# Kernel optimization log

Hardware: AMD Instinct MI355X
Metric: run time of the kernel (lower is better)

## Reference

```python
import jax, jax.numpy as jnp
import numpy as np

NV, NE = 4096, 8192
FV, FE = 128, 64
FV_OUT = 128


def setup_inputs() -> dict:
    key = jax.random.key(0)
    ks = jax.random.split(key, 8)
    stdv = 1.0 / np.sqrt(FV_OUT)
    return {
        "H_v": jax.random.normal(ks[0], (NV, FV), dtype=jnp.float32),
        "H_e": jax.random.normal(ks[1], (NE, FE), dtype=jnp.float32),
        "adj_e": jax.random.uniform(ks[2], (NE, NE), dtype=jnp.float32),
        "adj_v": jax.random.uniform(ks[3], (NV, NV), dtype=jnp.float32),
        "T": jax.random.uniform(ks[4], (NV, NE), dtype=jnp.float32),
        "weight": jax.random.uniform(ks[5], (FV, FV_OUT), minval=-stdv, maxval=stdv, dtype=jnp.float32),
        "p": jax.random.normal(ks[6], (1, FE), dtype=jnp.float32),
        "bias": jax.random.uniform(ks[7], (FV_OUT,), minval=-stdv, maxval=stdv, dtype=jnp.float32),
    }


def reference(H_v, H_e, adj_e, adj_v, T, weight, p, bias):
    # node_layer=True path of GraphConvolution.forward
    # d = (H_e @ p.T) as a vector over edges; T @ diag(d) == T * d[None, :]
    d = (H_e @ p.T)[:, 0]                       # [Ne]
    multiplier = (T * d[None, :]) @ T.T         # [Nv, Nv]
    n = multiplier.shape[0]
    mask = jnp.eye(n, dtype=multiplier.dtype)   # eye mask: diag -> 1, off-diag -> multiplier
    M1 = mask + (1.0 - mask) * multiplier
    adjusted_A = M1 * adj_v                     # elementwise mask with dense adjacency
    output = adjusted_A @ (H_v @ weight) + bias # [Nv, Fv_out]
    return (output, H_e)
```

## Files before the change

kernel.cpp:

```cpp
#include <hip/hip_runtime.h>
#include <stdint.h>

#define NV 4096
#define NE 8192
#define FV 128
#define FE 64
#define FOUT 128

typedef unsigned short u16;
typedef __attribute__((ext_vector_type(8))) short short8;
typedef __attribute__((ext_vector_type(4))) float f32x4;
typedef __attribute__((ext_vector_type(4))) unsigned short u16x4;

__device__ __forceinline__ u16 f2bf(float f) {
  uint32_t u = __builtin_bit_cast(uint32_t, f);
  u += 0x7fffu + ((u >> 16) & 1u);
  return (u16)(u >> 16);
}
__device__ __forceinline__ float bf2f(u16 h) {
  return __builtin_bit_cast(float, (uint32_t)h << 16);
}

#define AS1(p) ((__attribute__((address_space(1))) void*)(void*)(p))
#define AS3(p) ((__attribute__((address_space(3))) void*)(p))

__global__ __launch_bounds__(256) void k_edge_dot(const float* __restrict__ He,
                                                  const float* __restrict__ p,
                                                  float* __restrict__ d) {
  const int lane = threadIdx.x & 63;
  const int gw = blockIdx.x * 4 + (threadIdx.x >> 6);
  const float pv = p[lane];
  for (int e = gw; e < NE; e += 512) {
    float v = He[(size_t)e * FE + lane] * pv;
    #pragma unroll
    for (int off = 32; off > 0; off >>= 1) v += __shfl_down(v, off);
    if (lane == 0) d[e] = v;
  }
}

__global__ __launch_bounds__(256) void k_convert(const float* __restrict__ T,
                                                 const float* __restrict__ d,
                                                 u16* __restrict__ Ta,
                                                 u16* __restrict__ Tb) {
  size_t idx = ((size_t)blockIdx.x * 256 + threadIdx.x) * 8;
  f32x4 t0 = *(const f32x4*)&T[idx];
  f32x4 t1 = *(const f32x4*)&T[idx + 4];
  int e = (int)(idx & (NE - 1));
  f32x4 d0 = *(const f32x4*)&d[e];
  f32x4 d1 = *(const f32x4*)&d[e + 4];
  short8 a, b;
  a[0] = (short)f2bf(t0.x * d0.x); a[1] = (short)f2bf(t0.y * d0.y);
  a[2] = (short)f2bf(t0.z * d0.z); a[3] = (short)f2bf(t0.w * d0.w);
  a[4] = (short)f2bf(t1.x * d1.x); a[5] = (short)f2bf(t1.y * d1.y);
  a[6] = (short)f2bf(t1.z * d1.z); a[7] = (short)f2bf(t1.w * d1.w);
  b[0] = (short)f2bf(t0.x); b[1] = (short)f2bf(t0.y);
  b[2] = (short)f2bf(t0.z); b[3] = (short)f2bf(t0.w);
  b[4] = (short)f2bf(t1.x); b[5] = (short)f2bf(t1.y);
  b[6] = (short)f2bf(t1.z); b[7] = (short)f2bf(t1.w);
  *(short8*)&Ta[idx] = a;
  *(short8*)&Tb[idx] = b;
}

__global__ __launch_bounds__(256) void k_hw(const float* __restrict__ Hv,
                                            const float* __restrict__ W,
                                            u16* __restrict__ HWt) {
  __shared__ float sW[FV * FOUT];
  __shared__ float sH[8 * FV];
  const int tid = threadIdx.x;
  const int i0 = blockIdx.x * 8;
  #pragma unroll
  for (int k = 0; k < 16; ++k)
    *(f32x4*)&sW[k * 1024 + tid * 4] = *(const f32x4*)&W[k * 1024 + tid * 4];
  *(f32x4*)&sH[tid * 4] = *(const f32x4*)&Hv[(size_t)i0 * FV + tid * 4];
  __syncthreads();
  const int n = tid & 127;
  const int rh = tid >> 7;
  float acc[4] = {0.f, 0.f, 0.f, 0.f};
  #pragma unroll 4
  for (int f = 0; f < FV; ++f) {
    float wv = sW[f * FOUT + n];
    #pragma unroll
    for (int rr = 0; rr < 4; ++rr)
      acc[rr] += sH[(rh * 4 + rr) * FV + f] * wv;
  }
  #pragma unroll
  for (int rr = 0; rr < 4; ++rr)
    HWt[(size_t)n * NV + i0 + rh * 4 + rr] = f2bf(acc[rr]);
}

__global__ __launch_bounds__(256) void k_copy_he(float* __restrict__ out,
                                                 const float* __restrict__ He) {
  size_t idx = ((size_t)blockIdx.x * 256 + threadIdx.x) * 4;
  *(f32x4*)&out[(size_t)NV * FOUT + idx] = *(const f32x4*)&He[idx];
}

__global__ __launch_bounds__(512, 2) void k_gemm_m(const u16* __restrict__ Ta,
                                                   const u16* __restrict__ Tb,
                                                   const float* __restrict__ adjv,
                                                   u16* __restrict__ adjA) {
  __shared__ __align__(16) u16 smem[66560];

  const int bi = blockIdx.x >> 4;
  const int bj = blockIdx.x & 15;
  const int tile_m = bi * 256;
  const int tile_n = bj * 256;
  const int tid = threadIdx.x;
  const int lane = tid & 63;
  const int wid = tid >> 6;
  const int wr = wid >> 2;
  const int wc = wid & 3;
  const int row16 = lane & 15;
  const int quad = lane >> 4;
  const int swz8 = (quad ^ ((row16 >> 1) & 3)) * 8;

  const int srow = tid >> 2;
  const int sslot = (tid & 3) ^ ((tid >> 3) & 3);
  const u16* gA0 = Ta + (size_t)(tile_m + srow) * NE + sslot * 8;
  const u16* gA1 = gA0 + (size_t)128 * NE;
  const u16* gB0 = Tb + (size_t)(tile_n + srow) * NE + sslot * 8;
  const u16* gB1 = gB0 + (size_t)128 * NE;
  const int ldsO0 = (wid * 64) * 8;
  const int ldsO1 = (512 + wid * 64) * 8;

#define STG(gp0, gp1, roff, kcol)                                                                 \
  do {                                                                                            \
    __builtin_amdgcn_global_load_lds(AS1((gp0) + (kcol)), AS3(&smem[(roff) + ldsO0]), 16, 0, 0);  \
    __builtin_amdgcn_global_load_lds(AS1((gp1) + (kcol)), AS3(&smem[(roff) + ldsO1]), 16, 0, 0);  \
  } while (0)

  f32x4 acc[8][4] = {};
  short8 aF[4], bF[4];

  const int arow32 = (wr * 128 + row16) * 32 + swz8;
  const int brow32 = (wc * 64 + row16) * 32 + swz8;

#define LDA4(b, kk, mh)                                                                        \
  do { _Pragma("unroll")                                                                       \
    for (int m2 = 0; m2 < 4; ++m2)                                                             \
      aF[m2] = *(const short8*)&smem[(b)*16384 + (kk)*8192 + arow32 + ((mh)*4 + m2) * 512];    \
  } while (0)

#define LDB4(b, kk)                                                                            \
  do { _Pragma("unroll")                                                                       \
    for (int ni = 0; ni < 4; ++ni)                                                             \
      bF[ni] = *(const short8*)&smem[32768 + (b)*16384 + (kk)*8192 + brow32 + ni * 512];       \
  } while (0)

#define MMH(mh)                                                                                             \
  do { _Pragma("unroll")                                                                                    \
    for (int m2 = 0; m2 < 4; ++m2) { _Pragma("unroll")                                                      \
      for (int ni = 0; ni < 4; ++ni)                                                                        \
        acc[(mh)*4+m2][ni] = __builtin_amdgcn_mfma_f32_16x16x32_bf16(aF[m2], bF[ni], acc[(mh)*4+m2][ni], 0,0,0); \
    }                                                                                                       \
  } while (0)

#define BAR()   __builtin_amdgcn_s_barrier()
#define LGKM0() do { asm volatile("s_waitcnt lgkmcnt(0)" ::: "memory"); \
                     __builtin_amdgcn_sched_barrier(0); } while (0)
#define VM6()   asm volatile("s_waitcnt vmcnt(6)" ::: "memory")
#define PRIO1() __builtin_amdgcn_s_setprio(1)
#define PRIO0() __builtin_amdgcn_s_setprio(0)

  STG(gA0, gA1, 0,     0);
  STG(gB0, gB1, 32768, 0);
  STG(gA0, gA1, 8192,  32);
  STG(gB0, gB1, 40960, 32);
  STG(gB0, gB1, 49152, 64);
  STG(gA0, gA1, 16384, 64);
  STG(gB0, gB1, 57344, 96);
  VM6();
  BAR();

  for (int it = 0; it < 64; ++it) {
    const int t = it * 2;
    const int k1 = (t + 1) * 64;
    const int k2 = (t + 2 < 128 ? t + 2 : 127) * 64;
    const int k3 = (t + 3 < 128 ? t + 3 : 127) * 64;

    LDB4(0, 0); LDA4(0, 0, 0);
    STG(gA0, gA1, 24576, k1 + 32);
    BAR(); LGKM0();
    PRIO1(); MMH(0); PRIO0();
    BAR();

    LDA4(0, 0, 1);
    STG(gB0, gB1, 32768, k2);
    BAR(); LGKM0();
    PRIO1(); MMH(1); PRIO0();
    BAR();

    LDB4(0, 1); LDA4(0, 1, 0);
    STG(gA0, gA1, 0, k2);
    BAR(); LGKM0();
    PRIO1(); MMH(0); PRIO0();
    BAR();

    LDA4(0, 1, 1);
    STG(gB0, gB1, 40960, k2 + 32);
    BAR(); LGKM0();
    PRIO1(); MMH(1); PRIO0();
    VM6();
    BAR();

    LDB4(1, 0); LDA4(1, 0, 0);
    STG(gA0, gA1, 8192, k2 + 32);
    BAR(); LGKM0();
    PRIO1(); MMH(0); PRIO0();
    BAR();

    LDA4(1, 0, 1);
    STG(gB0, gB1, 49152, k3);
    BAR(); LGKM0();
    PRIO1(); MMH(1); PRIO0();
    BAR();

    LDB4(1, 1); LDA4(1, 1, 0);
    STG(gA0, gA1, 16384, k3);
    BAR(); LGKM0();
    PRIO1(); MMH(0); PRIO0();
    BAR();

    LDA4(1, 1, 1);
    STG(gB0, gB1, 57344, k3 + 32);
    BAR(); LGKM0();
    PRIO1(); MMH(1); PRIO0();
    VM6();
    BAR();
  }

  asm volatile("s_waitcnt vmcnt(0)" ::: "memory");
  __syncthreads();
  #pragma unroll
  for (int mi = 0; mi < 8; ++mi) {
    #pragma unroll
    for (int ni = 0; ni < 4; ++ni) {
      const int row = wr * 128 + mi * 16 + quad * 4;
      const int col = wc * 64 + ni * 16 + row16;
      #pragma unroll
      for (int r = 0; r < 4; ++r)
        smem[(row + r) * 260 + col] = f2bf(acc[mi][ni][r]);
    }
  }
  __syncthreads();
  const int ep_r = tid >> 4;
  const int ep_c = (tid & 15) * 4;
  for (int pass = 0; pass < 8; ++pass) {
    const int row = pass * 32 + ep_r;
    const int gr = tile_m + row;
    const size_t gbase = (size_t)gr * NV + tile_n;
    #pragma unroll
    for (int j = 0; j < 4; ++j) {
      const int col = ep_c + j * 64;
      const int gc = tile_n + col;
      u16x4 m4 = *(const u16x4*)&smem[row * 260 + col];
      f32x4 av = *(const f32x4*)&adjv[gbase + col];
      u16x4 o;
      o.x = f2bf(((gr == gc + 0) ? 1.0f : bf2f(m4.x)) * av.x);
      o.y = f2bf(((gr == gc + 1) ? 1.0f : bf2f(m4.y)) * av.y);
      o.z = f2bf(((gr == gc + 2) ? 1.0f : bf2f(m4.z)) * av.z);
      o.w = f2bf(((gr == gc + 3) ? 1.0f : bf2f(m4.w)) * av.w);
      *(u16x4*)&adjA[gbase + col] = o;
    }
  }

#undef STG
#undef LDA4
#undef LDB4
#undef MMH
#undef BAR
#undef LGKM0
#undef VM6
#undef PRIO1
#undef PRIO0
}

#define KSPLIT 16
__global__ __launch_bounds__(256) void k_gemm_out(const u16* __restrict__ A,
                                                  const u16* __restrict__ B,
                                                  float* __restrict__ part) {
  __shared__ __align__(16) u16 lA[128 * 32];
  __shared__ __align__(16) u16 lB[128 * 32];
  const int K = NV;
  const int tile_m = blockIdx.y * 128;
  const int kbeg = blockIdx.x * (K / KSPLIT);
  const int kend = kbeg + (K / KSPLIT);
  const int tid = threadIdx.x;
  const int lane = tid & 63;
  const int wave = tid >> 6;
  const int wm = (wave >> 1) * 64;
  const int wn = (wave & 1) * 64;
  const int row16 = lane & 15;
  const int quad = lane >> 4;

  f32x4 acc[4][4] = {};

  for (int k0 = kbeg; k0 < kend; k0 += 32) {
    __syncthreads();
    #pragma unroll
    for (int r = 0; r < 2; ++r) {
      const int chunk = r * 256 + wave * 64 + lane;
      const int row = chunk >> 2;
      const int cc = chunk & 3;
      const u16* ga = A + ((size_t)(tile_m + row) * K + k0 + cc * 8);
      const u16* gb = B + ((size_t)row * K + k0 + cc * 8);
      __builtin_amdgcn_global_load_lds(AS1(ga), AS3(&lA[(r * 256 + wave * 64) * 8]), 16, 0, 0);
      __builtin_amdgcn_global_load_lds(AS1(gb), AS3(&lB[(r * 256 + wave * 64) * 8]), 16, 0, 0);
    }
    __syncthreads();
    short8 a[4], b[4];
    #pragma unroll
    for (int mi = 0; mi < 4; ++mi)
      a[mi] = *(const short8*)&lA[(wm + mi * 16 + row16) * 32 + quad * 8];
    #pragma unroll
    for (int ni = 0; ni < 4; ++ni)
      b[ni] = *(const short8*)&lB[(wn + ni * 16 + row16) * 32 + quad * 8];
    #pragma unroll
    for (int mi = 0; mi < 4; ++mi)
      #pragma unroll
      for (int ni = 0; ni < 4; ++ni)
        acc[mi][ni] = __builtin_amdgcn_mfma_f32_16x16x32_bf16(a[mi], b[ni], acc[mi][ni], 0, 0, 0);
  }

  float* pdst = part + (size_t)blockIdx.x * NV * FOUT;
  #pragma unroll
  for (int mi = 0; mi < 4; ++mi) {
    #pragma unroll
    for (int ni = 0; ni < 4; ++ni) {
      const int gc = wn + ni * 16 + row16;
      #pragma unroll
      for (int r = 0; r < 4; ++r) {
        const int gr = tile_m + wm + mi * 16 + quad * 4 + r;
        pdst[(size_t)gr * FOUT + gc] = acc[mi][ni][r];
      }
    }
  }
}

__global__ __launch_bounds__(256) void k_reduce(const float* __restrict__ part,
                                                const float* __restrict__ bias,
                                                float* __restrict__ out) {
  size_t idx = ((size_t)blockIdx.x * 256 + threadIdx.x) * 4;
  f32x4 s = *(const f32x4*)&bias[idx & (FOUT - 1)];
  #pragma unroll
  for (int ks = 0; ks < KSPLIT; ++ks)
    s += *(const f32x4*)&part[(size_t)ks * NV * FOUT + idx];
  *(f32x4*)&out[idx] = s;
}

extern "C" void kernel_launch(void* const* d_in, const int* in_sizes, int n_in,
                              void* d_out, int out_size, void* d_ws, size_t ws_size,
                              hipStream_t stream) {
  const float* Hv   = (const float*)d_in[0];
  const float* He   = (const float*)d_in[1];
  const float* adjv = (const float*)d_in[3];
  const float* T    = (const float*)d_in[4];
  const float* W    = (const float*)d_in[5];
  const float* p    = (const float*)d_in[6];
  const float* bias = (const float*)d_in[7];
  float* out = (float*)d_out;

  char* ws = (char*)d_ws;
  float* dvec = (float*)ws;
  u16* HWt    = (u16*)(ws + ((size_t)1 << 20));
  u16* Ta     = (u16*)(ws + ((size_t)2 << 20));
  u16* Tb     = (u16*)(ws + ((size_t)2 << 20) + ((size_t)64 << 20));
  u16* adjA   = (u16*)(ws + ((size_t)2 << 20) + ((size_t)128 << 20));
  float* part = (float*)(ws + ((size_t)2 << 20) + ((size_t)160 << 20));

  k_edge_dot<<<128, 256, 0, stream>>>(He, p, dvec);
  k_convert<<<(NV * NE) / (256 * 8), 256, 0, stream>>>(T, dvec, Ta, Tb);
  k_hw<<<NV / 8, 256, 0, stream>>>(Hv, W, HWt);
  k_copy_he<<<(NE * FE) / (256 * 4), 256, 0, stream>>>(out, He);
  k_gemm_m<<<256, 512, 0, stream>>>(Ta, Tb, adjv, adjA);
  k_gemm_out<<<dim3(KSPLIT, NV / 128), 256, 0, stream>>>(adjA, HWt, part);
  k_reduce<<<(NV * FOUT) / (256 * 4), 256, 0, stream>>>(part, bias, out);
}
```

Measured before the change: 688.9 us.

## Double-buffer MFMA fragments in main GEMM, fuse H_e copy, halve split-K

The main 4096x4096x8192 bf16 GEMM now keeps two register sets of A/B fragments and prefetches the next LDS fragments while the current MFMAs run. It replaces full lgkmcnt(0) waits and double barriers with partial lgkmcnt waits and one barrier per phase. Separately, the H_e passthrough copy is folded into the edge-dot kernel, which removes a launch, and the output GEMM's split-K factor drops from 16 to 8. These trade extra register pressure and tighter wait-count bookkeeping for less LDS-latency stall and less launch and reduction overhead.

New measurement: 674.7 us. -2.1%, faster.

```diff
diff --git a/kernel.cpp b/kernel.cpp
--- a/kernel.cpp
+++ b/kernel.cpp
@@ -26,12 +26,15 @@
 
 __global__ __launch_bounds__(256) void k_edge_dot(const float* __restrict__ He,
                                                   const float* __restrict__ p,
-                                                  float* __restrict__ d) {
+                                                  float* __restrict__ d,
+                                                  float* __restrict__ out) {
   const int lane = threadIdx.x & 63;
   const int gw = blockIdx.x * 4 + (threadIdx.x >> 6);
   const float pv = p[lane];
   for (int e = gw; e < NE; e += 512) {
-    float v = He[(size_t)e * FE + lane] * pv;
+    float h = He[(size_t)e * FE + lane];
+    out[(size_t)NV * FOUT + (size_t)e * FE + lane] = h;
+    float v = h * pv;
     #pragma unroll
     for (int off = 32; off > 0; off >>= 1) v += __shfl_down(v, off);
     if (lane == 0) d[e] = v;
@@ -88,12 +91,6 @@
     HWt[(size_t)n * NV + i0 + rh * 4 + rr] = f2bf(acc[rr]);
 }
 
-__global__ __launch_bounds__(256) void k_copy_he(float* __restrict__ out,
-                                                 const float* __restrict__ He) {
-  size_t idx = ((size_t)blockIdx.x * 256 + threadIdx.x) * 4;
-  *(f32x4*)&out[(size_t)NV * FOUT + idx] = *(const f32x4*)&He[idx];
-}
-
 __global__ __launch_bounds__(512, 2) void k_gemm_m(const u16* __restrict__ Ta,
                                                    const u16* __restrict__ Tb,
                                                    const float* __restrict__ adjv,
@@ -129,106 +126,107 @@
   } while (0)
 
   f32x4 acc[8][4] = {};
-  short8 aF[4], bF[4];
+  short8 aX[4], aY[4], bX[4], bY[4];
 
   const int arow32 = (wr * 128 + row16) * 32 + swz8;
   const int brow32 = (wc * 64 + row16) * 32 + swz8;
 
-#define LDA4(b, kk, mh)                                                                        \
+#define LDSA(b, kk, mh, DST)                                                                   \
   do { _Pragma("unroll")                                                                       \
     for (int m2 = 0; m2 < 4; ++m2)                                                             \
-      aF[m2] = *(const short8*)&smem[(b)*16384 + (kk)*8192 + arow32 + ((mh)*4 + m2) * 512];    \
+      DST[m2] = *(const short8*)&smem[(b)*16384 + (kk)*8192 + arow32 + ((mh)*4 + m2) * 512];   \
   } while (0)
 
-#define LDB4(b, kk)                                                                            \
+#define LDSB(b, kk, DST)                                                                       \
   do { _Pragma("unroll")                                                                       \
     for (int ni = 0; ni < 4; ++ni)                                                             \
-      bF[ni] = *(const short8*)&smem[32768 + (b)*16384 + (kk)*8192 + brow32 + ni * 512];       \
+      DST[ni] = *(const short8*)&smem[32768 + (b)*16384 + (kk)*8192 + brow32 + ni * 512];      \
   } while (0)
 
-#define MMH(mh)                                                                                             \
+#define MMP(mh, ASET, BSET)                                                                                 \
   do { _Pragma("unroll")                                                                                    \
     for (int m2 = 0; m2 < 4; ++m2) { _Pragma("unroll")                                                      \
       for (int ni = 0; ni < 4; ++ni)                                                                        \
-        acc[(mh)*4+m2][ni] = __builtin_amdgcn_mfma_f32_16x16x32_bf16(aF[m2], bF[ni], acc[(mh)*4+m2][ni], 0,0,0); \
+        acc[(mh)*4+m2][ni] = __builtin_amdgcn_mfma_f32_16x16x32_bf16(ASET[m2], BSET[ni], acc[(mh)*4+m2][ni], 0,0,0); \
     }                                                                                                       \
   } while (0)
 
-#define BAR()   __builtin_amdgcn_s_barrier()
-#define LGKM0() do { asm volatile("s_waitcnt lgkmcnt(0)" ::: "memory"); \
-                     __builtin_amdgcn_sched_barrier(0); } while (0)
-#define VM6()   asm volatile("s_waitcnt vmcnt(6)" ::: "memory")
+#define BARF()  do { __builtin_amdgcn_s_barrier(); asm volatile("" ::: "memory"); } while (0)
+#define WAITK(k) do { asm volatile("s_waitcnt lgkmcnt(" #k ")" ::: "memory"); \
+                      __builtin_amdgcn_sched_barrier(0); } while (0)
+#define GATE8() asm volatile("s_waitcnt vmcnt(8)" ::: "memory")
 #define PRIO1() __builtin_amdgcn_s_setprio(1)
 #define PRIO0() __builtin_amdgcn_s_setprio(0)
 
+  STG(gB0, gB1, 32768, 0);
   STG(gA0, gA1, 0,     0);
-  STG(gB0, gB1, 32768, 0);
+  STG(gB0, gB1, 40960, 32);
   STG(gA0, gA1, 8192,  32);
-  STG(gB0, gB1, 40960, 32);
   STG(gB0, gB1, 49152, 64);
   STG(gA0, gA1, 16384, 64);
   STG(gB0, gB1, 57344, 96);
-  VM6();
-  BAR();
-
+  asm volatile("s_waitcnt vmcnt(10)" ::: "memory");
+  BARF();
+  LDSB(0, 0, bX);
+  LDSA(0, 0, 0, aX);
+
+  #pragma unroll 1
   for (int it = 0; it < 64; ++it) {
     const int t = it * 2;
     const int k1 = (t + 1) * 64;
     const int k2 = (t + 2 < 128 ? t + 2 : 127) * 64;
     const int k3 = (t + 3 < 128 ? t + 3 : 127) * 64;
 
-    LDB4(0, 0); LDA4(0, 0, 0);
+    LDSA(0, 0, 1, aY);
     STG(gA0, gA1, 24576, k1 + 32);
-    BAR(); LGKM0();
-    PRIO1(); MMH(0); PRIO0();
-    BAR();
-
-    LDA4(0, 0, 1);
+    WAITK(4);
+    PRIO1(); MMP(0, aX, bX); PRIO0();
+    GATE8(); BARF();
+
+    LDSB(0, 1, bY); LDSA(0, 1, 0, aX);
     STG(gB0, gB1, 32768, k2);
-    BAR(); LGKM0();
-    PRIO1(); MMH(1); PRIO0();
-    BAR();
-
-    LDB4(0, 1); LDA4(0, 1, 0);
+    WAITK(8);
+    PRIO1(); MMP(1, aY, bX); PRIO0();
+    BARF();
+
+    LDSA(0, 1, 1, aY);
     STG(gA0, gA1, 0, k2);
-    BAR(); LGKM0();
-    PRIO1(); MMH(0); PRIO0();
-    BAR();
-
-    LDA4(0, 1, 1);
+    WAITK(4);
+    PRIO1(); MMP(0, aX, bY); PRIO0();
+    GATE8(); BARF();
+
+    LDSB(1, 0, bX); LDSA(1, 0, 0, aX);
     STG(gB0, gB1, 40960, k2 + 32);
-    BAR(); LGKM0();
-    PRIO1(); MMH(1); PRIO0();
-    VM6();
-    BAR();
-
-    LDB4(1, 0); LDA4(1, 0, 0);
+    WAITK(8);
+    PRIO1(); MMP(1, aY, bY); PRIO0();
+    BARF();
+
+    LDSA(1, 0, 1, aY);
     STG(gA0, gA1, 8192, k2 + 32);
-    BAR(); LGKM0();
-    PRIO1(); MMH(0); PRIO0();
-    BAR();
-
-    LDA4(1, 0, 1);
+    WAITK(4);
+    PRIO1(); MMP(0, aX, bX); PRIO0();
+    GATE8(); BARF();
+
+    LDSB(1, 1, bY); LDSA(1, 1, 0, aX);
     STG(gB0, gB1, 49152, k3);
-    BAR(); LGKM0();
-    PRIO1(); MMH(1); PRIO0();
-    BAR();
-
-    LDB4(1, 1); LDA4(1, 1, 0);
+    WAITK(8);
+    PRIO1(); MMP(1, aY, bX); PRIO0();
+    BARF();
+
+    LDSA(1, 1, 1, aY);
     STG(gA0, gA1, 16384, k3);
-    BAR(); LGKM0();
-    PRIO1(); MMH(0); PRIO0();
-    BAR();
-
-    LDA4(1, 1, 1);
+    WAITK(4);
+    PRIO1(); MMP(0, aX, bY); PRIO0();
+    GATE8(); BARF();
+
+    LDSB(0, 0, bX); LDSA(0, 0, 0, aX);
     STG(gB0, gB1, 57344, k3 + 32);
-    BAR(); LGKM0();
-    PRIO1(); MMH(1); PRIO0();
-    VM6();
-    BAR();
-  }
-
-  asm volatile("s_waitcnt vmcnt(0)" ::: "memory");
+    WAITK(8);
+    PRIO1(); MMP(1, aY, bY); PRIO0();
+    BARF();
+  }
+
+  asm volatile("s_waitcnt vmcnt(0) lgkmcnt(0)" ::: "memory");
   __syncthreads();
   #pragma unroll
   for (int mi = 0; mi < 8; ++mi) {
@@ -264,17 +262,17 @@
   }
 
 #undef STG
-#undef LDA4
-#undef LDB4
-#undef MMH
-#undef BAR
-#undef LGKM0
-#undef VM6
+#undef LDSA
+#undef LDSB
+#undef MMP
+#undef BARF
+#undef WAITK
+#undef GATE8
 #undef PRIO1
 #undef PRIO0
 }
 
-#define KSPLIT 16
+#define KSPLIT 8
 __global__ __launch_bounds__(256) void k_gemm_out(const u16* __restrict__ A,
                                                   const u16* __restrict__ B,
                                                   float* __restrict__ part) {
@@ -367,10 +365,9 @@
   u16* adjA   = (u16*)(ws + ((size_t)2 << 20) + ((size_t)128 << 20));
   float* part = (float*)(ws + ((size_t)2 << 20) + ((size_t)160 << 20));
 
-  k_edge_dot<<<128, 256, 0, stream>>>(He, p, dvec);
+  k_edge_dot<<<128, 256, 0, stream>>>(He, p, dvec, out);
   k_convert<<<(NV * NE) / (256 * 8), 256, 0, stream>>>(T, dvec, Ta, Tb);
   k_hw<<<NV / 8, 256, 0, stream>>>(Hv, W, HWt);
-  k_copy_he<<<(NE * FE) / (256 * 4), 256, 0, stream>>>(out, He);
   k_gemm_m<<<256, 512, 0, stream>>>(Ta, Tb, adjv, adjA);
   k_gemm_out<<<dim3(KSPLIT, NV / 128), 256, 0, stream>>>(adjA, HWt, part);
   k_reduce<<<(NV * FOUT) / (256 * 4), 256, 0, stream>>>(part, bias, out);
```
